# Performance work log

Hardware: AMD Instinct MI355X
Metric: run time of the kernel (lower is better)

## Reference

```python
import jax, jax.numpy as jnp
import numpy as np

# static config matching init_kwargs
IN_SIZE = 128
OUT_SIZE = 128
KSIZE = 3
POS = 10
DIL = 1
B = 8
L = 8192


def setup_inputs() -> dict:
    key = jax.random.key(0)
    k1, k2, k3, k4, k5 = jax.random.split(key, 5)
    inputs = jax.random.normal(k1, (B, IN_SIZE, L), dtype=jnp.float32)
    connections = jax.random.randint(k2, (B, L), 0, L)  # indices into length axis
    mask = jax.random.randint(k3, (B, L), 0, 2).astype(bool)
    ch_in = (2 * IN_SIZE + POS) * KSIZE  # 798
    W = jax.random.normal(k4, (OUT_SIZE, ch_in), dtype=jnp.float32) / np.float32(np.sqrt(ch_in))
    b = jax.random.normal(k5, (OUT_SIZE,), dtype=jnp.float32) * 0.01
    return {"inputs": inputs, "connections": connections, "mask": mask, "W": W, "b": b}


def reference(inputs, connections, mask, W, b):
    Bn, C, Ln = inputs.shape
    # gather neighbor features: out[b,c,l] = inputs[b,c,connections[b,l]]  -> [B,C,L]
    conn_vals = jnp.take_along_axis(inputs, connections[:, None, :], axis=2)
    # trig positional encoding of relative offsets  -> [B,POS,L]
    pos = jnp.arange(Ln, dtype=jnp.float32)[None]              # [1,L]
    delta = (pos - connections.astype(jnp.float32))[:, None, :]  # [B,1,L]
    scales = (2.0 ** jnp.arange(POS, dtype=jnp.float32))[None, :, None]
    penc = jnp.sin(scales * delta / 1000.0)
    out = jnp.concatenate([inputs, conn_vals, penc], axis=1)   # [B, 2C+POS, L]
    # non-causal pad + unfold (window KSIZE, step 1); num windows == L
    pad = KSIZE * DIL // 2
    out = jnp.pad(out, ((0, 0), (0, 0), (pad, pad)))
    # build [B, Ch, KSIZE, L]: window k is out_padded[..., k : k+L]
    out = jnp.stack([out[..., k:k + Ln] for k in range(KSIZE)], axis=2)
    out = out.reshape(Bn, -1, Ln)                               # [B, Ch*KSIZE, L]
    # 1x1 conv == per-position GEMM
    y = jnp.einsum('oc,bcl->bol', W, out) + b[None, :, None]    # [B, OUT, L]
    return y * mask[:, None, :].astype(y.dtype)
```

## Files before the change

### kernel.cpp

```cpp
#include <hip/hip_runtime.h>
#include <math.h>

#define B_    8
#define C_    128
#define L_    8192
#define O_    128
#define POS_  10
#define CHIN  798
#define CH_   266
#define GSTR  128
#define NCH   9
#define TL2   128
#define G_ELEMS  ((size_t)B_ * L_ * GSTR)
#define WT_ELEMS ((size_t)3 * NCH * O_ * 32)

typedef _Float16 half8 __attribute__((ext_vector_type(8)));
typedef short short8 __attribute__((ext_vector_type(8)));
typedef float f32x4  __attribute__((ext_vector_type(4)));

typedef __attribute__((address_space(3))) unsigned       lds_uint;
typedef __attribute__((address_space(1))) const unsigned gl_uint;

__device__ __forceinline__ void dma16(const _Float16* g, _Float16* l) {
    __builtin_amdgcn_global_load_lds((gl_uint*)g, (lds_uint*)l, 16, 0, 0);
}

__device__ __forceinline__ void detect_core(const uint4* __restrict__ m,
                                            int* __restrict__ mflag, int tid) {
    __shared__ int s[2];
    if (tid < 2) s[tid] = 0;
    __syncthreads();
    unsigned sub = 0, mid = 0;
    #pragma unroll
    for (int k = 0; k < 16; ++k) {
        uint4 w = m[tid + k * 256];
        sub |= (w.x | w.y | w.z | w.w) & 0xFFFFFF00u;
        mid |= (w.y | w.w) & 0x000000FFu;
    }
    unsigned long long bs = __ballot(sub != 0);
    unsigned long long bm = __ballot(mid != 0);
    if ((tid & 63) == 0) {
        if (bs) atomicOr(&s[0], 1);
        if (bm) atomicOr(&s[1], 1);
    }
    __syncthreads();
    if (tid == 0) mflag[0] = s[0] ? 1 : (s[1] ? 0 : 2);
}

__global__ void detect_kernel(const uint4* __restrict__ m, int* __restrict__ mflag) {
    detect_core(m, mflag, threadIdx.x);
}

__global__ __launch_bounds__(256, 4)
void prep_kernel(const float* __restrict__ inputs, const float* __restrict__ W,
                 const uint4* __restrict__ maskv,
                 _Float16* __restrict__ G, _Float16* __restrict__ Wt2,
                 int* __restrict__ mflag) {
    __shared__ float tile[64][65];
    const int bid = blockIdx.x;
    const int tid = threadIdx.x;

    if (bid == 2480) { detect_core(maskv, mflag, tid); return; }

    if (bid >= 2048) {
        int idx = (bid - 2048) * 256 + tid;
        int cc  = idx & 31;
        int o   = (idx >> 5) & 127;
        int tch = idx >> 12;
        int ch  = tch % 9;
        int t   = tch / 9;
        int cg  = ch * 32 + cc;
        Wt2[idx] = (cg < CH_) ? (_Float16)W[o * CHIN + 3 * cg + t] : (_Float16)0.f;
        return;
    }

    const int b  = bid & 7;
    const int r  = bid >> 3;
    const int c0 = (r & 1) * 64;
    const int l0 = (r >> 1) * 64;
    const int ty = tid >> 6, tx = tid & 63;

    #pragma unroll
    for (int it = 0; it < 16; ++it) {
        int cl = it * 4 + ty;
        tile[cl][tx] = inputs[((size_t)(b * C_ + c0 + cl)) * L_ + l0 + tx];
    }
    __syncthreads();
    const int cp = (tid & 31) * 2;
    const int lr = tid >> 5;
    #pragma unroll
    for (int it = 0; it < 8; ++it) {
        int ll = it * 8 + lr;
        _Float16 pair[2] = {(_Float16)tile[cp][ll], (_Float16)tile[cp + 1][ll]};
        *(unsigned*)&G[((size_t)(b * L_ + l0 + ll)) * GSTR + c0 + cp] = *(unsigned*)pair;
    }
}

__global__ __launch_bounds__(256)
void k2_gemm(const _Float16* __restrict__ G, const _Float16* __restrict__ Wt2,
             const int* __restrict__ conn,
             const unsigned char* __restrict__ mask,
             const float* __restrict__ bias,
             float* __restrict__ out,
             const int* __restrict__ mflag_p) {
    __shared__ _Float16 As[2][3][128][32];
    __shared__ _Float16 Bs[2][130][32];
    __shared__ int conn_s[130];

    const int bid = blockIdx.x;
    const int b   = bid & 7;
    const int l0  = (bid >> 3) * TL2;
    const int tid  = threadIdx.x;
    const int wave = tid >> 6;
    const int lane = tid & 63;
    const int wo = wave & 1;
    const int wl = wave >> 1;
    const int g  = lane >> 4;
    const int ln = lane & 15;

    const _Float16* gb = G + (size_t)b * L_ * GSTR;

    for (int j = tid; j < TL2 + 2; j += 256) {
        int l_ = l0 - 1 + j;
        conn_s[j] = ((unsigned)l_ < (unsigned)L_) ? conn[b * L_ + l_] : 0;
    }

    const int ra  = 1 + 32 * wave + (lane >> 2);
    const int cja = conn[b * L_ + l0 - 1 + ra];
    const int cjb = conn[b * L_ + l0 - 1 + ra + 16];
    const int cbl = lane & 3;

    auto stage_dma = [&](int ch, int buf) {
        #pragma unroll
        for (int i = 0; i < 6; ++i) {
            int ap = 6 * wave + i;
            int tp = ap >> 3;
            int og = ap & 7;
            int o  = og * 16 + (lane >> 2);
            const _Float16* src = &Wt2[((size_t)((tp * NCH + ch) * O_ + o)) * 32 + cbl * 8];
            dma16(src, &As[buf][tp][og * 16][0]);
        }
        #pragma unroll
        for (int i = 0; i < 2; ++i) {
            int r0 = 1 + 32 * wave + 16 * i;
            const _Float16* src;
            if (ch < 4) {
                int r = r0 + (lane >> 2);
                src = &gb[(size_t)(l0 - 1 + r) * GSTR + ch * 32 + cbl * 8];
            } else {
                int cj = i ? cjb : cja;
                src = &gb[(size_t)cj * GSTR + (ch - 4) * 32 + cbl * 8];
            }
            dma16(src, &Bs[buf][r0][0]);
        }
    };
    auto stage_dma_a_only = [&](int ch, int buf) {
        #pragma unroll
        for (int i = 0; i < 6; ++i) {
            int ap = 6 * wave + i;
            int tp = ap >> 3;
            int og = ap & 7;
            int o  = og * 16 + (lane >> 2);
            const _Float16* src = &Wt2[((size_t)((tp * NCH + ch) * O_ + o)) * 32 + cbl * 8];
            dma16(src, &As[buf][tp][og * 16][0]);
        }
    };

    auto halo_load = [&](int ch) -> short8 {
        int row = (tid >> 2) ? 129 : 0;
        int l_  = l0 - 1 + row;
        short8 v = (short8)0;
        if ((unsigned)l_ < (unsigned)L_) {
            if (ch < 4) {
                v = *(const short8*)&gb[(size_t)l_ * GSTR + ch * 32 + (tid & 3) * 8];
            } else {
                int cj = conn_s[row];
                v = *(const short8*)&gb[(size_t)cj * GSTR + (ch - 4) * 32 + (tid & 3) * 8];
            }
        }
        return v;
    };
    auto halo_write = [&](short8 v, int buf) {
        int row = (tid >> 2) ? 129 : 0;
        *(short8*)&Bs[buf][row][(tid & 3) * 8] = v;
    };

    auto penc_val = [&](int q) -> short8 {
        int cb = q & 3, j = q >> 2;
        int l_ = l0 - 1 + j;
        short8 v = (short8)0;
        if ((unsigned)l_ < (unsigned)L_ && cb < 2) {
            float d = (float)(l_ - conn_s[j]);
            _Float16 h[8];
            #pragma unroll
            for (int e = 0; e < 8; ++e) {
                int p = cb * 8 + e;
                h[e] = (p < POS_) ? (_Float16)sinf(((float)(1 << p)) * d / 1000.0f)
                                  : (_Float16)0.f;
            }
            v = *(short8*)h;
        }
        return v;
    };

#define PENC_WR(BUF) { { int cb_ = tid & 3, j_ = tid >> 2; \
            *(short8*)&Bs[BUF][j_][cb_ * 8] = s0; } \
        { int q_ = tid + 256; int cb_ = q_ & 3, j_ = q_ >> 2; \
            *(short8*)&Bs[BUF][j_][cb_ * 8] = s1; } \
        if (tid < 8) { int q_ = 512 + tid; int cb_ = q_ & 3, j_ = q_ >> 2; \
            *(short8*)&Bs[BUF][j_][cb_ * 8] = s2; } }

#define COMPUTE(BUF) { _Pragma("unroll") for (int t_ = 0; t_ < 3; ++t_) { \
        half8 bf_[4]; \
        _Pragma("unroll") for (int n_ = 0; n_ < 4; ++n_) \
            bf_[n_] = *(const half8*)&Bs[BUF][wl * 64 + n_ * 16 + ln + t_][8 * g]; \
        _Pragma("unroll") for (int m_ = 0; m_ < 4; ++m_) { \
            half8 af_ = *(const half8*)&As[BUF][t_][wo * 64 + m_ * 16 + ln][8 * g]; \
            _Pragma("unroll") for (int n_ = 0; n_ < 4; ++n_) \
                acc[m_][n_] = __builtin_amdgcn_mfma_f32_16x16x32_f16(af_, bf_[n_], acc[m_][n_], 0, 0, 0); } } }

    f32x4 acc[4][4];
    #pragma unroll
    for (int m = 0; m < 4; ++m)
        #pragma unroll
        for (int n = 0; n < 4; ++n) acc[m][n] = (f32x4)0.f;

    short8 s0, s1, s2, hv;

    stage_dma(0, 0);
    if (tid < 8) { hv = halo_load(0); halo_write(hv, 0); }
    __syncthreads();

    for (int ch = 0; ch < 8; ch += 2) {
        stage_dma(ch + 1, 1);
        if (tid < 8) hv = halo_load(ch + 1);
        COMPUTE(0);
        if (tid < 8) halo_write(hv, 1);
        __syncthreads();

        if (ch + 2 == 8) {
            stage_dma_a_only(8, 0);
            s0 = penc_val(tid); s1 = penc_val(tid + 256);
            if (tid < 8) s2 = penc_val(512 + tid);
            COMPUTE(1);
            PENC_WR(0);
        } else {
            stage_dma(ch + 2, 0);
            if (tid < 8) hv = halo_load(ch + 2);
            COMPUTE(1);
            if (tid < 8) halo_write(hv, 0);
        }
        __syncthreads();
    }
    COMPUTE(0);

    const int mflag = mflag_p[0];
    float mv[4];
    #pragma unroll
    for (int n = 0; n < 4; ++n) {
        int l = l0 + wl * 64 + n * 16 + ln;
        int idx = b * L_ + l;
        if (mflag == 1)      mv[n] = mask[idx] ? 1.f : 0.f;
        else if (mflag == 0) mv[n] = ((const int*)mask)[idx] ? 1.f : 0.f;
        else                 mv[n] = ((const int*)mask)[2 * idx] ? 1.f : 0.f;
    }
    #pragma unroll
    for (int m = 0; m < 4; ++m) {
        #pragma unroll
        for (int r = 0; r < 4; ++r) {
            int o = wo * 64 + m * 16 + g * 4 + r;
            float bo = bias[o];
            #pragma unroll
            for (int n = 0; n < 4; ++n) {
                int l = l0 + wl * 64 + n * 16 + ln;
                out[((size_t)(b * O_ + o)) * L_ + l] = (acc[m][n][r] + bo) * mv[n];
            }
        }
    }
#undef PENC_WR
#undef COMPUTE
}

__global__ __launch_bounds__(256, 2)
void cc_fallback_kernel(const float* __restrict__ inputs,
                        const int* __restrict__ conn,
                        const unsigned char* __restrict__ mask,
                        const float* __restrict__ W,
                        const float* __restrict__ bias,
                        float* __restrict__ out,
                        const int* __restrict__ mflag_p) {
    __shared__ int   conn_s[130];
    __shared__ float feat_s[16][132];
    __shared__ float Ws[48][136];

    const int b   = blockIdx.y;
    const int l0  = blockIdx.x * 128;
    const int tid = threadIdx.x;
    const int ot  = tid >> 4;
    const int lt  = tid & 15;
    const int o0  = ot * 8;
    const int ll  = lt * 8;

    for (int j = tid; j < 130; j += 256) {
        int lg = l0 - 1 + j;
        conn_s[j] = ((unsigned)lg < (unsigned)L_) ? conn[b * L_ + lg] : -1;
    }
    float acc[8][8];
    #pragma unroll
    for (int i = 0; i < 8; ++i)
        #pragma unroll
        for (int j = 0; j < 8; ++j) acc[i][j] = 0.f;

    const int tc = ot, tj = lt;
    for (int chunk = 0; chunk < 17; ++chunk) {
        const int CN  = (chunk < 16) ? 16 : POS_;
        const int cg0 = chunk * 16;
        const int col0 = 3 * cg0;
        __syncthreads();
        {
            const int nw = O_ * CN * 3;
            for (int idx = tid; idx < nw; idx += 256) {
                int o = idx & 127, kk = idx >> 7;
                Ws[kk][o] = W[o * CHIN + col0 + kk];
            }
        }
        if (chunk < 8) {
            const float* src = inputs + ((size_t)b * C_ + (cg0 + tc)) * L_;
            for (int j = tj; j < 130; j += 16) {
                int lg = l0 - 1 + j;
                feat_s[tc][j] = ((unsigned)lg < (unsigned)L_) ? src[lg] : 0.f;
            }
        } else if (chunk < 16) {
            const float* src = inputs + ((size_t)b * C_ + (cg0 - 128 + tc)) * L_;
            for (int j = tj; j < 130; j += 16) {
                int cj = conn_s[j];
                feat_s[tc][j] = (cj >= 0) ? src[cj] : 0.f;
            }
        } else if (tc < POS_) {
            const float sc = (float)(1 << tc);
            for (int j = tj; j < 130; j += 16) {
                int cj = conn_s[j];
                int lg = l0 - 1 + j;
                float v = 0.f;
                if (cj >= 0) v = sinf((sc * (float)(lg - cj)) / 1000.0f);
                feat_s[tc][j] = v;
            }
        }
        __syncthreads();
        for (int c = 0; c < CN; ++c) {
            float f[10];
            float4 fa = *(const float4*)&feat_s[c][ll];
            float4 fb = *(const float4*)&feat_s[c][ll + 4];
            float2 fc2 = *(const float2*)&feat_s[c][ll + 8];
            f[0]=fa.x; f[1]=fa.y; f[2]=fa.z; f[3]=fa.w;
            f[4]=fb.x; f[5]=fb.y; f[6]=fb.z; f[7]=fb.w;
            f[8]=fc2.x; f[9]=fc2.y;
            #pragma unroll
            for (int k = 0; k < 3; ++k) {
                const float* wrow = &Ws[c * 3 + k][o0];
                float4 wa = *(const float4*)&wrow[0];
                float4 wb = *(const float4*)&wrow[4];
                float w[8] = {wa.x, wa.y, wa.z, wa.w, wb.x, wb.y, wb.z, wb.w};
                #pragma unroll
                for (int oi = 0; oi < 8; ++oi)
                    #pragma unroll
                    for (int li = 0; li < 8; ++li)
                        acc[oi][li] = fmaf(w[oi], f[li + k], acc[oi][li]);
            }
        }
    }
    const int mflag = mflag_p[0];
    const int lbase = l0 + ll;
    float mv[8];
    #pragma unroll
    for (int li = 0; li < 8; ++li) {
        int idx = b * L_ + lbase + li;
        if (mflag == 1)      mv[li] = mask[idx] ? 1.f : 0.f;
        else if (mflag == 0) mv[li] = ((const int*)mask)[idx] ? 1.f : 0.f;
        else                 mv[li] = ((const int*)mask)[2 * idx] ? 1.f : 0.f;
    }
    #pragma unroll
    for (int oi = 0; oi < 8; ++oi) {
        float bo = bias[o0 + oi];
        float* dst = out + ((size_t)b * O_ + o0 + oi) * L_ + lbase;
        #pragma unroll
        for (int li = 0; li < 8; ++li) dst[li] = (acc[oi][li] + bo) * mv[li];
    }
}

extern "C" void kernel_launch(void* const* d_in, const int* in_sizes, int n_in,
                              void* d_out, int out_size, void* d_ws, size_t ws_size,
                              hipStream_t stream) {
    const float*         inputs = (const float*)d_in[0];
    const int*           conn   = (const int*)d_in[1];
    const unsigned char* mask   = (const unsigned char*)d_in[2];
    const float*         W      = (const float*)d_in[3];
    const float*         bias   = (const float*)d_in[4];
    float*               out    = (float*)d_out;

    const size_t g_bytes  = G_ELEMS * sizeof(_Float16);
    const size_t wt_bytes = WT_ELEMS * sizeof(_Float16);
    const size_t need     = g_bytes + wt_bytes + 64;

    if (ws_size < need) {
        int* mflag = (int*)d_ws;
        detect_kernel<<<1, 256, 0, stream>>>((const uint4*)mask, mflag);
        dim3 grid(L_ / 128, B_);
        cc_fallback_kernel<<<grid, 256, 0, stream>>>(inputs, conn, mask, W, bias, out, mflag);
        return;
    }

    _Float16* G     = (_Float16*)d_ws;
    _Float16* Wt2   = (_Float16*)((char*)d_ws + g_bytes);
    int*      mflag = (int*)((char*)d_ws + g_bytes + wt_bytes);

    prep_kernel<<<2481, 256, 0, stream>>>(inputs, W, (const uint4*)mask, G, Wt2, mflag);
    k2_gemm<<<512, 256, 0, stream>>>(G, Wt2, conn, mask, bias, out, mflag);
}
```

Before: 51.43 us.

## Materialize gathered features and positional encoding in a separate pre-pass kernel

Adds a kernel that writes the gathered neighbor features and the sinusoidal positional encoding into a widened fp16 feature buffer (row stride grows from 128 to 288). The GEMM kernel can then stream all nine channel chunks contiguously by row, without indirect per-row DMA addresses, the conn table in shared memory, or sinf work inside the main loop. The cost is an extra kernel launch, more than double the buffer footprint, and an extra write-then-read pass over the gathered data in global memory.

```diff
diff --git a/kernel.cpp b/kernel.cpp
--- a/kernel.cpp
+++ b/kernel.cpp
@@ -8,10 +8,10 @@
 #define POS_  10
 #define CHIN  798
 #define CH_   266
-#define GSTR  128
+#define GS    288
 #define NCH   9
 #define TL2   128
-#define G_ELEMS  ((size_t)B_ * L_ * GSTR)
+#define G_ELEMS  ((size_t)B_ * L_ * GS)
 #define WT_ELEMS ((size_t)3 * NCH * O_ * 32)
 
 typedef _Float16 half8 __attribute__((ext_vector_type(8)));
@@ -92,20 +92,52 @@
     for (int it = 0; it < 8; ++it) {
         int ll = it * 8 + lr;
         _Float16 pair[2] = {(_Float16)tile[cp][ll], (_Float16)tile[cp + 1][ll]};
-        *(unsigned*)&G[((size_t)(b * L_ + l0 + ll)) * GSTR + c0 + cp] = *(unsigned*)pair;
+        *(unsigned*)&G[((size_t)(b * L_ + l0 + ll)) * GS + c0 + cp] = *(unsigned*)pair;
+    }
+}
+
+__global__ __launch_bounds__(256, 4)
+void k1_gather_penc(const int* __restrict__ conn, _Float16* __restrict__ G) {
+    const int bid = blockIdx.x;
+    const int b  = bid & 7;
+    const int l0 = (bid >> 3) * 64;
+    const int tid = threadIdx.x;
+    const int wv = tid >> 6, lane = tid & 63;
+
+    #pragma unroll
+    for (int i = 0; i < 8; ++i) {
+        int l  = l0 + wv * 16 + i * 2 + (lane >> 5);
+        int cj = conn[b * L_ + l];
+        uint2 v = *(const uint2*)&G[((size_t)(b * L_ + cj)) * GS + (lane & 31) * 4];
+        *(uint2*)&G[((size_t)(b * L_ + l)) * GS + 128 + (lane & 31) * 4] = v;
+    }
+
+    {
+        int l = l0 + (tid >> 2);
+        int s = tid & 3;
+        int cj = conn[b * L_ + l];
+        float d = (float)(l - cj);
+        _Float16 v[8];
+        #pragma unroll
+        for (int e = 0; e < 8; ++e) {
+            int p = s * 8 + e;
+            if (p < POS_) {
+                float sc = (float)(1 << p);
+                v[e] = (_Float16)sinf((sc * d) / 1000.0f);
+            } else v[e] = (_Float16)0.f;
+        }
+        *(short8*)&G[((size_t)(b * L_ + l)) * GS + 256 + s * 8] = *(short8*)v;
     }
 }
 
 __global__ __launch_bounds__(256)
 void k2_gemm(const _Float16* __restrict__ G, const _Float16* __restrict__ Wt2,
-             const int* __restrict__ conn,
              const unsigned char* __restrict__ mask,
              const float* __restrict__ bias,
              float* __restrict__ out,
              const int* __restrict__ mflag_p) {
     __shared__ _Float16 As[2][3][128][32];
     __shared__ _Float16 Bs[2][130][32];
-    __shared__ int conn_s[130];
 
     const int bid = blockIdx.x;
     const int b   = bid & 7;
@@ -118,16 +150,7 @@
     const int g  = lane >> 4;
     const int ln = lane & 15;
 
-    const _Float16* gb = G + (size_t)b * L_ * GSTR;
-
-    for (int j = tid; j < TL2 + 2; j += 256) {
-        int l_ = l0 - 1 + j;
-        conn_s[j] = ((unsigned)l_ < (unsigned)L_) ? conn[b * L_ + l_] : 0;
-    }
-
-    const int ra  = 1 + 32 * wave + (lane >> 2);
-    const int cja = conn[b * L_ + l0 - 1 + ra];
-    const int cjb = conn[b * L_ + l0 - 1 + ra + 16];
+    const _Float16* gb = G + (size_t)b * L_ * GS;
     const int cbl = lane & 3;
 
     auto stage_dma = [&](int ch, int buf) {
@@ -143,26 +166,9 @@
         #pragma unroll
         for (int i = 0; i < 2; ++i) {
             int r0 = 1 + 32 * wave + 16 * i;
-            const _Float16* src;
-            if (ch < 4) {
-                int r = r0 + (lane >> 2);
-                src = &gb[(size_t)(l0 - 1 + r) * GSTR + ch * 32 + cbl * 8];
-            } else {
-                int cj = i ? cjb : cja;
-                src = &gb[(size_t)cj * GSTR + (ch - 4) * 32 + cbl * 8];
-            }
+            int r  = r0 + (lane >> 2);
+            const _Float16* src = &gb[(size_t)(l0 - 1 + r) * GS + ch * 32 + cbl * 8];
             dma16(src, &Bs[buf][r0][0]);
-        }
-    };
-    auto stage_dma_a_only = [&](int ch, int buf) {
-        #pragma unroll
-        for (int i = 0; i < 6; ++i) {
-            int ap = 6 * wave + i;
-            int tp = ap >> 3;
-            int og = ap & 7;
-            int o  = og * 16 + (lane >> 2);
-            const _Float16* src = &Wt2[((size_t)((tp * NCH + ch) * O_ + o)) * 32 + cbl * 8];
-            dma16(src, &As[buf][tp][og * 16][0]);
         }
     };
 
@@ -170,45 +176,14 @@
         int row = (tid >> 2) ? 129 : 0;
         int l_  = l0 - 1 + row;
         short8 v = (short8)0;
-        if ((unsigned)l_ < (unsigned)L_) {
-            if (ch < 4) {
-                v = *(const short8*)&gb[(size_t)l_ * GSTR + ch * 32 + (tid & 3) * 8];
-            } else {
-                int cj = conn_s[row];
-                v = *(const short8*)&gb[(size_t)cj * GSTR + (ch - 4) * 32 + (tid & 3) * 8];
-            }
-        }
+        if ((unsigned)l_ < (unsigned)L_)
+            v = *(const short8*)&gb[(size_t)l_ * GS + ch * 32 + (tid & 3) * 8];
         return v;
     };
     auto halo_write = [&](short8 v, int buf) {
         int row = (tid >> 2) ? 129 : 0;
         *(short8*)&Bs[buf][row][(tid & 3) * 8] = v;
     };
-
-    auto penc_val = [&](int q) -> short8 {
-        int cb = q & 3, j = q >> 2;
-        int l_ = l0 - 1 + j;
-        short8 v = (short8)0;
-        if ((unsigned)l_ < (unsigned)L_ && cb < 2) {
-            float d = (float)(l_ - conn_s[j]);
-            _Float16 h[8];
-            #pragma unroll
-            for (int e = 0; e < 8; ++e) {
-                int p = cb * 8 + e;
-                h[e] = (p < POS_) ? (_Float16)sinf(((float)(1 << p)) * d / 1000.0f)
-                                  : (_Float16)0.f;
-            }
-            v = *(short8*)h;
-        }
-        return v;
-    };
-
-#define PENC_WR(BUF) { { int cb_ = tid & 3, j_ = tid >> 2; \
-            *(short8*)&Bs[BUF][j_][cb_ * 8] = s0; } \
-        { int q_ = tid + 256; int cb_ = q_ & 3, j_ = q_ >> 2; \
-            *(short8*)&Bs[BUF][j_][cb_ * 8] = s1; } \
-        if (tid < 8) { int q_ = 512 + tid; int cb_ = q_ & 3, j_ = q_ >> 2; \
-            *(short8*)&Bs[BUF][j_][cb_ * 8] = s2; } }
 
 #define COMPUTE(BUF) { _Pragma("unroll") for (int t_ = 0; t_ < 3; ++t_) { \
         half8 bf_[4]; \
@@ -225,7 +200,7 @@
         #pragma unroll
         for (int n = 0; n < 4; ++n) acc[m][n] = (f32x4)0.f;
 
-    short8 s0, s1, s2, hv;
+    short8 hv;
 
     stage_dma(0, 0);
     if (tid < 8) { hv = halo_load(0); halo_write(hv, 0); }
@@ -238,18 +213,10 @@
         if (tid < 8) halo_write(hv, 1);
         __syncthreads();
 
-        if (ch + 2 == 8) {
-            stage_dma_a_only(8, 0);
-            s0 = penc_val(tid); s1 = penc_val(tid + 256);
-            if (tid < 8) s2 = penc_val(512 + tid);
-            COMPUTE(1);
-            PENC_WR(0);
-        } else {
-            stage_dma(ch + 2, 0);
-            if (tid < 8) hv = halo_load(ch + 2);
-            COMPUTE(1);
-            if (tid < 8) halo_write(hv, 0);
-        }
+        stage_dma(ch + 2, 0);
+        if (tid < 8) hv = halo_load(ch + 2);
+        COMPUTE(1);
+        if (tid < 8) halo_write(hv, 0);
         __syncthreads();
     }
     COMPUTE(0);
@@ -277,7 +244,6 @@
             }
         }
     }
-#undef PENC_WR
 #undef COMPUTE
 }
 
@@ -415,5 +381,6 @@
     int*      mflag = (int*)((char*)d_ws + g_bytes + wt_bytes);
 
     prep_kernel<<<2481, 256, 0, stream>>>(inputs, W, (const uint4*)mask, G, Wt2, mflag);
-    k2_gemm<<<512, 256, 0, stream>>>(G, Wt2, conn, mask, bias, out, mflag);
-}
+    k1_gather_penc<<<1024, 256, 0, stream>>>(conn, G);
+    k2_gemm<<<512, 256, 0, stream>>>(G, Wt2, mask, bias, out, mflag);
+}
```

Result: faster. 43.51 us (-15.4%).
